# Kernel optimization log

Hardware: AMD Instinct MI355X
Metric: run time of the kernel (lower is better)

## Reference

```python
import jax, jax.numpy as jnp
import numpy as np

B, C, H, W, K = 4, 64, 128, 128, 3
K2 = K * K
PAD = (K - 1) // 2  # same padding for 3x3


def setup_inputs() -> dict:
    key = jax.random.key(0)
    ks = jax.random.split(key, 9)
    s = 0.05
    return {
        "x": jax.random.normal(ks[0], (B, C, H, W), jnp.float32),
        "inter": jax.random.normal(ks[1], (B, C, H, W), jnp.float32),
        # offset/mask predictor conv: input cat([x, inter]) -> 3*K2 channels (dy, dx, mask)
        "w_offset": jax.random.normal(ks[2], (3 * K2, 2 * C, K, K), jnp.float32) * s,
        "b_offset": jnp.zeros((3 * K2,), jnp.float32),
        # deformable conv weight (bias=False per DGM init)
        "w_dcn": jax.random.normal(ks[3], (C, C, K, K), jnp.float32) * s,
        # SFT gamma branch: two 1x1 convs (bias=False)
        "w_g1": jax.random.normal(ks[4], (C, C), jnp.float32) * s,
        "w_g2": jax.random.normal(ks[5], (C, C), jnp.float32) * s,
        # SFT beta branch: two 1x1 convs (bias=False)
        "w_b1": jax.random.normal(ks[6], (C, C), jnp.float32) * s,
        "w_b2": jax.random.normal(ks[7], (C, C), jnp.float32) * s,
    }


def _lrelu(v):
    # LeakyReLU(0.1)
    return jnp.where(v >= 0, v, 0.1 * v)


def _conv(x, w, b=None):
    y = jax.lax.conv_general_dilated(
        x, w, window_strides=(1, 1), padding=[(PAD, PAD), (PAD, PAD)],
        dimension_numbers=("NCHW", "OIHW", "NCHW"))
    if b is not None:
        y = y + b[None, :, None, None]
    return y


def _bilinear_gather(x, py, px):
    """x: [B,C,H,W]; py, px: [B,K2,H,W] float sample coords.
    Returns samples [B,K2,H,W,C]; out-of-bounds treated as zero (DCN zero-pad)."""
    y0 = jnp.floor(py)
    x0 = jnp.floor(px)
    wy = (py - y0)[..., None]
    wx = (px - x0)[..., None]

    def gather(yi, xi):
        valid = ((yi >= 0) & (yi < H) & (xi >= 0) & (xi < W)).astype(x.dtype)
        yc = jnp.clip(yi, 0, H - 1).astype(jnp.int32)
        xc = jnp.clip(xi, 0, W - 1).astype(jnp.int32)
        bidx = jnp.arange(B)[:, None, None, None]
        v = x[bidx, :, yc, xc]  # advanced indexing -> [B,K2,H,W,C]
        return v * valid[..., None]

    v00 = gather(y0, x0)
    v01 = gather(y0, x0 + 1)
    v10 = gather(y0 + 1, x0)
    v11 = gather(y0 + 1, x0 + 1)
    return (v00 * (1 - wy) * (1 - wx) + v01 * (1 - wy) * wx
            + v10 * wy * (1 - wx) + v11 * wy * wx)


def _dgm_forward(x, inter, w_offset, b_offset, w_dcn, w_g1, w_g2, w_b1, w_b2):
    # --- WADCN branch: modulated deformable conv, offsets predicted from cat(x, inter)
    om = _conv(jnp.concatenate([x, inter], axis=1), w_offset, b_offset)  # [B,3K2,H,W]
    dy, dx, m = jnp.split(om, 3, axis=1)  # each [B,K2,H,W]
    mask = jax.nn.sigmoid(m)

    ky, kx = jnp.meshgrid(jnp.arange(K), jnp.arange(K), indexing="ij")
    ky = ky.reshape(K2).astype(x.dtype)
    kx = kx.reshape(K2).astype(x.dtype)
    hh = jnp.arange(H, dtype=x.dtype)
    ww = jnp.arange(W, dtype=x.dtype)
    # sample coords: base grid + kernel-tap offset + learned offset
    py = hh[None, None, :, None] + (ky - PAD)[None, :, None, None] + dy  # [B,K2,H,W]
    px = ww[None, None, None, :] + (kx - PAD)[None, :, None, None] + dx

    samp = _bilinear_gather(x, py, px) * mask[..., None]  # [B,K2,H,W,C]
    dcn_out = jnp.einsum("bkhwc,ock->bohw", samp, w_dcn.reshape(C, C, K2))

    # --- SFT branch: two 1x1-conv + LeakyReLU chains producing gamma/beta
    gamma = jnp.einsum("oc,bchw->bohw", w_g2,
                       _lrelu(jnp.einsum("oc,bchw->bohw", w_g1, inter)))
    beta = jnp.einsum("oc,bchw->bohw", w_b2,
                      _lrelu(jnp.einsum("oc,bchw->bohw", w_b1, inter)))
    sft_out = x * gamma + beta

    # --- fused residual combine (DGM.relu is defined but never applied)
    return x + dcn_out + sft_out


def reference(x, inter, w_offset, b_offset, w_dcn, w_g1, w_g2, w_b1, w_b2):
    return _dgm_forward(x, inter, w_offset, b_offset, w_dcn, w_g1, w_g2, w_b1, w_b2)
```

## Files before the change

### kernel.cpp

```cpp
#include <hip/hip_runtime.h>
#include <hip/hip_bf16.h>
#include <math.h>

#define BB 4
#define CC 64
#define HH 128
#define WW 128
#define HW (HH*WW)
#define NPIX (BB*HW)

typedef __attribute__((ext_vector_type(8))) short short8;
typedef __attribute__((ext_vector_type(4))) float f32x4;

__device__ __forceinline__ float bf2f(ushort u) {
  union { unsigned u; float f; } v; v.u = ((unsigned)u) << 16; return v.f;
}
__device__ __forceinline__ ushort f2bf(float f) {
  __hip_bfloat16 h = __float2bfloat16(f); return *(ushort*)&h;
}

__global__ __launch_bounds__(256) void k_prep(
    const float* __restrict__ x, const float* __restrict__ inter,
    const float* __restrict__ w_off, const float* __restrict__ w_dcn,
    const float* __restrict__ wg1, const float* __restrict__ wb1,
    const float* __restrict__ wg2, const float* __restrict__ wb2,
    ushort* __restrict__ x_clh, ushort* __restrict__ inter_clh,
    ushort* __restrict__ wfb, ushort* __restrict__ wdT,
    ushort* __restrict__ w1gb, ushort* __restrict__ w1bb,
    ushort* __restrict__ w2gb, ushort* __restrict__ w2bb,
    float* __restrict__ zp) {
  __shared__ float tile[64 * 129];
  int blk = blockIdx.x;
  if (blk < 1024) {
    int sel = blk >> 9;
    int bh = blk & 511;
    int b = bh >> 7, h = bh & 127;
    const float* src = sel ? inter : x;
    ushort* dst = sel ? inter_clh : x_clh;
    const float* sp = src + (size_t)(b * 64) * HW + h * WW;
    for (int i = threadIdx.x; i < 64 * 128; i += 256) {
      int c = i >> 7, w = i & 127;
      tile[c * 129 + w] = sp[(size_t)c * HW + w];
    }
    __syncthreads();
    ushort* dp = dst + ((size_t)b * HW + h * WW) * 64;
    for (int i = threadIdx.x; i < 64 * 128; i += 256) {
      int w = i >> 6, c = i & 63;
      dp[w * 64 + c] = f2bf(tile[c * 129 + w]);
    }
  } else if (blk < 1168) {
    int i = (blk - 1024) * 256 + threadIdx.x;
    if (i < 64) zp[i] = 0.f;
    if (i < 9 * 32 * 128) {
      int tap = i >> 12, rem = i & 4095, m = rem >> 7, c = rem & 127;
      float v = (m < 27) ? w_off[(size_t)(m * 128 + c) * 9 + tap] : 0.f;
      wfb[i] = f2bf(v);
    }
  } else if (blk < 1312) {
    int i = (blk - 1168) * 256 + threadIdx.x;
    if (i < 64 * 64 * 9) {
      int o = i / 576, rem = i % 576, k = rem >> 6, c = rem & 63;
      wdT[i] = f2bf(w_dcn[(o * 64 + c) * 9 + k]);
    }
  } else {
    int i = (blk - 1312) * 256 + threadIdx.x;
    int m = i >> 12, j = i & 4095;
    const float* src = (m == 0) ? wg1 : (m == 1) ? wb1 : (m == 2) ? wg2 : wb2;
    ushort* dst = (m == 0) ? w1gb : (m == 1) ? w1bb : (m == 2) ? w2gb : w2bb;
    dst[j] = f2bf(src[j]);
  }
}

#define CPITCH 72
#define SPITCH 200
#define NPX 32
#define FPX 72

__global__ __launch_bounds__(256) void k_omega(
    const float* __restrict__ x, const ushort* __restrict__ x_clh,
    const ushort* __restrict__ inter_clh,
    const float* __restrict__ b_off, const ushort* __restrict__ wfb,
    const ushort* __restrict__ wdT,
    const ushort* __restrict__ w1gb, const ushort* __restrict__ w1bb,
    const ushort* __restrict__ w2gb, const ushort* __restrict__ w2bb,
    const ushort* __restrict__ zp16, float* __restrict__ out) {
  __shared__ __align__(16) ushort BIGB[6 * 34 * CPITCH];
  __shared__ float oml[28 * 33];
  ushort* S  = BIGB;
  ushort* Sg = BIGB + 6400;
  ushort* Sb = Sg + NPX * FPX;
  int*   cy  = (int*)(BIGB + 6400);
  int*   cx  = cy + 288;
  float* cwy = (float*)(cx + 288);
  float* cwx = cwy + 288;
  float* cm  = cwx + 288;

  int tid = threadIdx.x;
  int wave = tid >> 6, lane = tid & 63;
  int quad = lane >> 4, col = lane & 15;
  int rr = lane >> 3, g = lane & 7;
  int pg0 = blockIdx.x * NPX;
  int b = pg0 >> 14, hw0 = pg0 & 16383;
  int h = hw0 >> 7, w0 = hw0 & 127;
  int pt = wave >> 1, mt = wave & 1;
  int o_base = __builtin_amdgcn_readfirstlane(wave * 16);

  {
    int ch = (tid & 7) * 8;
    unsigned bbase = (unsigned)b * HW;
#pragma unroll
    for (int it = 0; it < 7; ++it) {
      int e = it * 32 + (tid >> 3);
      if (e < 204) {
        int srcrow = e / 34, pxl = e % 34;
        int src = srcrow / 3, row = srcrow % 3;
        int hs = h + row - 1;
        int ps = w0 + pxl - 1;
        bool ok = ((unsigned)hs < 128u) && ((unsigned)ps < 128u);
        int hc = hs < 0 ? 0 : (hs > 127 ? 127 : hs);
        int pc = ps < 0 ? 0 : (ps > 127 ? 127 : ps);
        const ushort* sb = src ? inter_clh : x_clh;
        short8 v = *(const short8*)(sb + ((size_t)(bbase + (hc << 7) + pc)) * 64 + ch);
        short8 z = {0, 0, 0, 0, 0, 0, 0, 0};
        if (!ok) v = z;
        *(short8*)(&BIGB[e * CPITCH + ch]) = v;
      }
    }
  }
  __syncthreads();

  {
    f32x4 accx = {0.f, 0.f, 0.f, 0.f}, acci = {0.f, 0.f, 0.f, 0.f};
    const ushort* wb0 = wfb + (size_t)(mt * 16 + col) * 128 + quad * 8;
    int pxb = pt * 16 + col;
#pragma unroll
    for (int ky = 0; ky < 3; ++ky) {
#pragma unroll
      for (int kx = 0; kx < 3; ++kx) {
        int tap = ky * 3 + kx;
        const ushort* wt = wb0 + (size_t)tap * 4096;
#pragma unroll
        for (int ks = 0; ks < 2; ++ks) {
          short8 a0 = *(const short8*)(wt + ks * 32);
          short8 b0 = *(const short8*)(&BIGB[(ky * 34 + pxb + kx) * CPITCH + ks * 32 + quad * 8]);
          accx = __builtin_amdgcn_mfma_f32_16x16x32_bf16(a0, b0, accx, 0, 0, 0);
          short8 a1 = *(const short8*)(wt + 64 + ks * 32);
          short8 b1 = *(const short8*)(&BIGB[((3 + ky) * 34 + pxb + kx) * CPITCH + ks * 32 + quad * 8]);
          acci = __builtin_amdgcn_mfma_f32_16x16x32_bf16(a1, b1, acci, 0, 0, 0);
        }
      }
    }
#pragma unroll
    for (int r = 0; r < 4; ++r) {
      int o = mt * 16 + quad * 4 + r;
      if (o < 27) oml[o * 33 + pt * 16 + col] = accx[r] + acci[r];
    }
  }
  __syncthreads();

  f32x4 ag[2], ab[2];
#pragma unroll
  for (int nt = 0; nt < 2; ++nt) {
    ag[nt] = (f32x4){0.f, 0.f, 0.f, 0.f};
    ab[nt] = (f32x4){0.f, 0.f, 0.f, 0.f};
  }
#pragma unroll
  for (int ks = 0; ks < 2; ++ks) {
    short8 a_g = *(const short8*)(w1gb + (size_t)(o_base + col) * 64 + ks * 32 + quad * 8);
    short8 a_b = *(const short8*)(w1bb + (size_t)(o_base + col) * 64 + ks * 32 + quad * 8);
#pragma unroll
    for (int nt = 0; nt < 2; ++nt) {
      short8 bf = *(const short8*)(inter_clh + (size_t)(pg0 + nt * 16 + col) * 64 + ks * 32 + quad * 8);
      ag[nt] = __builtin_amdgcn_mfma_f32_16x16x32_bf16(a_g, bf, ag[nt], 0, 0, 0);
      ab[nt] = __builtin_amdgcn_mfma_f32_16x16x32_bf16(a_b, bf, ab[nt], 0, 0, 0);
    }
  }
#pragma unroll
  for (int nt = 0; nt < 2; ++nt) {
    int px = nt * 16 + col;
    ushort pkg[4], pkb[4];
#pragma unroll
    for (int r = 0; r < 4; ++r) {
      float vg = ag[nt][r]; vg = vg >= 0.f ? vg : 0.1f * vg;
      float vb = ab[nt][r]; vb = vb >= 0.f ? vb : 0.1f * vb;
      pkg[r] = f2bf(vg); pkb[r] = f2bf(vb);
    }
    *(uint2*)(&Sg[px * FPX + o_base + quad * 4]) = *(uint2*)pkg;
    *(uint2*)(&Sb[px * FPX + o_base + quad * 4]) = *(uint2*)pkb;
  }
  __syncthreads();

  f32x4 gg[2], gb[2];
#pragma unroll
  for (int nt = 0; nt < 2; ++nt) {
    gg[nt] = (f32x4){0.f, 0.f, 0.f, 0.f};
    gb[nt] = (f32x4){0.f, 0.f, 0.f, 0.f};
  }
#pragma unroll
  for (int ks = 0; ks < 2; ++ks) {
    short8 a_g = *(const short8*)(w2gb + (size_t)(o_base + col) * 64 + ks * 32 + quad * 8);
    short8 a_b = *(const short8*)(w2bb + (size_t)(o_base + col) * 64 + ks * 32 + quad * 8);
#pragma unroll
    for (int nt = 0; nt < 2; ++nt) {
      short8 bgf = *(const short8*)(Sg + (nt * 16 + col) * FPX + ks * 32 + quad * 8);
      short8 bbf = *(const short8*)(Sb + (nt * 16 + col) * FPX + ks * 32 + quad * 8);
      gg[nt] = __builtin_amdgcn_mfma_f32_16x16x32_bf16(a_g, bgf, gg[nt], 0, 0, 0);
      gb[nt] = __builtin_amdgcn_mfma_f32_16x16x32_bf16(a_b, bbf, gb[nt], 0, 0, 0);
    }
  }
  float xv[2][4];
#pragma unroll
  for (int nt = 0; nt < 2; ++nt)
#pragma unroll
    for (int r = 0; r < 4; ++r) {
      int o = o_base + quad * 4 + r;
      xv[nt][r] = x[(size_t)(b * 64 + o) * HW + hw0 + nt * 16 + col];
    }
  __syncthreads();

  for (int i = tid; i < 9 * NPX; i += 256) {
    int k = i >> 5, p = i & 31;
    float dy = oml[k * 33 + p] + b_off[k];
    float dx = oml[(9 + k) * 33 + p] + b_off[9 + k];
    float mz = oml[(18 + k) * 33 + p] + b_off[18 + k];
    float py = (float)(h + (k / 3) - 1) + dy;
    float px = (float)(w0 + p + (k % 3) - 1) + dx;
    float y0f = floorf(py), x0f = floorf(px);
    cy[i] = (int)y0f;
    cx[i] = (int)x0f;
    cwy[i] = py - y0f;
    cwx[i] = px - x0f;
    cm[i] = 1.f / (1.f + __expf(-mz));
  }

  f32x4 acc[2];
  acc[0] = (f32x4){0.f, 0.f, 0.f, 0.f};
  acc[1] = (f32x4){0.f, 0.f, 0.f, 0.f};

  const ushort* bp = x_clh + (size_t)b * HW * 64;

  for (int chunk = 0; chunk < 3; ++chunk) {
    __syncthreads();
#pragma unroll
    for (int it = 0; it < 3; ++it) {
      int p = wave * 8 + rr;
      int idx = (chunk * 3 + it) * NPX + p;
      int y0 = cy[idx], x0 = cx[idx];
      float wy = cwy[idx], wx = cwx[idx], m = cm[idx];
      bool yok0 = (unsigned)y0 < 128u, yok1 = (unsigned)(y0 + 1) < 128u;
      bool xok0 = (unsigned)x0 < 128u, xok1 = (unsigned)(x0 + 1) < 128u;
      const ushort* r0 = bp + ((size_t)(int)((y0 << 7) + x0)) * 64 + g * 8;
      const ushort* r1 = r0 + (size_t)WW * 64;
      short8 s00 = *(const short8*)((yok0 && xok0) ? r0 : zp16);
      short8 s01 = *(const short8*)((yok0 && xok1) ? (r0 + 64) : zp16);
      short8 s10 = *(const short8*)((yok1 && xok0) ? r1 : zp16);
      short8 s11 = *(const short8*)((yok1 && xok1) ? (r1 + 64) : zp16);
      short8 outv;
#pragma unroll
      for (int j = 0; j < 8; ++j) {
        float v00 = bf2f((ushort)s00[j]), v01 = bf2f((ushort)s01[j]);
        float v10 = bf2f((ushort)s10[j]), v11 = bf2f((ushort)s11[j]);
        float top = v00 + (v01 - v00) * wx;
        float bot = v10 + (v11 - v10) * wx;
        float val = top + (bot - top) * wy;
        outv[j] = (short)f2bf(val * m);
      }
      *(short8*)(&S[p * SPITCH + it * 64 + g * 8]) = outv;
    }
    __syncthreads();
    const ushort* wrow = wdT + (size_t)(o_base + col) * 576 + chunk * 192 + quad * 8;
    const ushort* srow = S + quad * 8;
#pragma unroll
    for (int ks = 0; ks < 6; ++ks) {
      short8 a = *(const short8*)(wrow + ks * 32);
#pragma unroll
      for (int nt = 0; nt < 2; ++nt) {
        short8 bf = *(const short8*)(srow + (nt * 16 + col) * SPITCH + ks * 32);
        acc[nt] = __builtin_amdgcn_mfma_f32_16x16x32_bf16(a, bf, acc[nt], 0, 0, 0);
      }
    }
  }

#pragma unroll
  for (int nt = 0; nt < 2; ++nt) {
#pragma unroll
    for (int r = 0; r < 4; ++r) {
      int o = o_base + quad * 4 + r;
      size_t idx = (size_t)(b * 64 + o) * HW + hw0 + nt * 16 + col;
      out[idx] = xv[nt][r] + xv[nt][r] * gg[nt][r] + gb[nt][r] + acc[nt][r];
    }
  }
}

extern "C" void kernel_launch(void* const* d_in, const int* in_sizes, int n_in,
                              void* d_out, int out_size, void* d_ws, size_t ws_size,
                              hipStream_t stream) {
  const float* x     = (const float*)d_in[0];
  const float* inter = (const float*)d_in[1];
  const float* w_off = (const float*)d_in[2];
  const float* b_off = (const float*)d_in[3];
  const float* w_dcn = (const float*)d_in[4];
  const float* wg1   = (const float*)d_in[5];
  const float* wg2   = (const float*)d_in[6];
  const float* wb1   = (const float*)d_in[7];
  const float* wb2   = (const float*)d_in[8];
  float* out = (float*)d_out;

  float* ws        = (float*)d_ws;
  ushort* x_clh    = (ushort*)ws;
  ushort* inter_clh= (ushort*)(ws + 2097152);
  ushort* wfb      = (ushort*)(ws + 5963776);
  ushort* wdT      = (ushort*)(ws + 5982208);
  ushort* w1gb     = (ushort*)(ws + 6000640);
  ushort* w1bb     = (ushort*)(ws + 6002688);
  ushort* w2gb     = (ushort*)(ws + 6004736);
  ushort* w2bb     = (ushort*)(ws + 6006784);
  float* zp        = ws + 6008832;

  k_prep<<<1376, 256, 0, stream>>>(x, inter, w_off, w_dcn, wg1, wb1, wg2, wb2,
                                   x_clh, inter_clh, wfb, wdT,
                                   w1gb, w1bb, w2gb, w2bb, zp);

  k_omega<<<2048, 256, 0, stream>>>(x, x_clh, inter_clh, b_off, wfb, wdT,
                                    w1gb, w1bb, w2gb, w2bb,
                                    (const ushort*)zp, out);
}
```

Baseline: 173.1 us.

## Vectorize prep transpose with swizzled LDS and alias offset buffer into shared tile

```diff
diff --git a/kernel.cpp b/kernel.cpp
--- a/kernel.cpp
+++ b/kernel.cpp
@@ -29,8 +29,9 @@
     ushort* __restrict__ w1gb, ushort* __restrict__ w1bb,
     ushort* __restrict__ w2gb, ushort* __restrict__ w2bb,
     float* __restrict__ zp) {
-  __shared__ float tile[64 * 129];
+  __shared__ __align__(16) float tile[64 * 128];
   int blk = blockIdx.x;
+  int tid = threadIdx.x;
   if (blk < 1024) {
     int sel = blk >> 9;
     int bh = blk & 511;
@@ -38,18 +39,32 @@
     const float* src = sel ? inter : x;
     ushort* dst = sel ? inter_clh : x_clh;
     const float* sp = src + (size_t)(b * 64) * HW + h * WW;
-    for (int i = threadIdx.x; i < 64 * 128; i += 256) {
-      int c = i >> 7, w = i & 127;
-      tile[c * 129 + w] = sp[(size_t)c * HW + w];
+#pragma unroll
+    for (int it = 0; it < 8; ++it) {
+      int idx = it * 256 + tid;
+      int c = idx >> 5, wq = idx & 31;
+      float4 v = *(const float4*)(sp + (size_t)c * HW + wq * 4);
+      int s = (c >> 3) & 7;
+      *(float4*)(&tile[c * 128 + ((wq ^ s) << 2)]) = v;
     }
     __syncthreads();
     ushort* dp = dst + ((size_t)b * HW + h * WW) * 64;
-    for (int i = threadIdx.x; i < 64 * 128; i += 256) {
-      int w = i >> 6, c = i & 63;
-      dp[w * 64 + c] = f2bf(tile[c * 129 + w]);
+#pragma unroll
+    for (int it = 0; it < 4; ++it) {
+      int idx = it * 256 + tid;
+      int w = idx >> 3, c8 = idx & 7;
+      short8 outv;
+#pragma unroll
+      for (int j = 0; j < 8; ++j) {
+        int c = c8 * 8 + j;
+        int sl = (w >> 2) ^ c8;
+        float f = tile[c * 128 + (sl << 2) + (w & 3)];
+        outv[j] = (short)f2bf(f);
+      }
+      *(short8*)(dp + (size_t)w * 64 + c8 * 8) = outv;
     }
   } else if (blk < 1168) {
-    int i = (blk - 1024) * 256 + threadIdx.x;
+    int i = (blk - 1024) * 256 + tid;
     if (i < 64) zp[i] = 0.f;
     if (i < 9 * 32 * 128) {
       int tap = i >> 12, rem = i & 4095, m = rem >> 7, c = rem & 127;
@@ -57,13 +72,13 @@
       wfb[i] = f2bf(v);
     }
   } else if (blk < 1312) {
-    int i = (blk - 1168) * 256 + threadIdx.x;
+    int i = (blk - 1168) * 256 + tid;
     if (i < 64 * 64 * 9) {
       int o = i / 576, rem = i % 576, k = rem >> 6, c = rem & 63;
       wdT[i] = f2bf(w_dcn[(o * 64 + c) * 9 + k]);
     }
   } else {
-    int i = (blk - 1312) * 256 + threadIdx.x;
+    int i = (blk - 1312) * 256 + tid;
     int m = i >> 12, j = i & 4095;
     const float* src = (m == 0) ? wg1 : (m == 1) ? wb1 : (m == 2) ? wg2 : wb2;
     ushort* dst = (m == 0) ? w1gb : (m == 1) ? w1bb : (m == 2) ? w2gb : w2bb;
@@ -85,7 +100,6 @@
     const ushort* __restrict__ w2gb, const ushort* __restrict__ w2bb,
     const ushort* __restrict__ zp16, float* __restrict__ out) {
   __shared__ __align__(16) ushort BIGB[6 * 34 * CPITCH];
-  __shared__ float oml[28 * 33];
   ushort* S  = BIGB;
   ushort* Sg = BIGB + 6400;
   ushort* Sb = Sg + NPX * FPX;
@@ -94,6 +108,7 @@
   float* cwy = (float*)(cx + 288);
   float* cwx = cwy + 288;
   float* cm  = cwx + 288;
+  float* oml = (float*)(BIGB + 11008);
 
   int tid = threadIdx.x;
   int wave = tid >> 6, lane = tid & 63;
@@ -129,8 +144,8 @@
   }
   __syncthreads();
 
+  f32x4 accx = {0.f, 0.f, 0.f, 0.f}, acci = {0.f, 0.f, 0.f, 0.f};
   {
-    f32x4 accx = {0.f, 0.f, 0.f, 0.f}, acci = {0.f, 0.f, 0.f, 0.f};
     const ushort* wb0 = wfb + (size_t)(mt * 16 + col) * 128 + quad * 8;
     int pxb = pt * 16 + col;
 #pragma unroll
@@ -150,13 +165,14 @@
         }
       }
     }
-#pragma unroll
-    for (int r = 0; r < 4; ++r) {
-      int o = mt * 16 + quad * 4 + r;
-      if (o < 27) oml[o * 33 + pt * 16 + col] = accx[r] + acci[r];
-    }
   }
   __syncthreads();
+
+#pragma unroll
+  for (int r = 0; r < 4; ++r) {
+    int o = mt * 16 + quad * 4 + r;
+    if (o < 27) oml[o * 33 + pt * 16 + col] = accx[r] + acci[r];
+  }
 
   f32x4 ag[2], ab[2];
 #pragma unroll
```

After: 169.6 us. 2.0% less time.
